# Optimization experiments

Hardware: AMD Instinct MI355X
Metric: run time of the kernel (lower is better)

Reference implementation:

```python
import jax, jax.numpy as jnp
import numpy as np


def setup_inputs() -> dict:
    key = jax.random.key(0)
    k1, k2, k3 = jax.random.split(key, 3)
    B, T, C, F = 32, 4096, 256, 256
    scale = 1.0 / np.sqrt(2 * C)  # glorot-ish fan-in scaling for kernel_size=2
    return {
        "x": jax.random.normal(k1, (B, T, C), dtype=jnp.float32),
        "Wv": jax.random.normal(k2, (2, C, F), dtype=jnp.float32) * scale,
        "bv": jnp.zeros((F,), dtype=jnp.float32),
        "Wg": jax.random.normal(k3, (2, C, F), dtype=jnp.float32) * scale,
        "bg": jnp.zeros((F,), dtype=jnp.float32),
        "dilation": 4,
    }


def _causal_dilated_k2(x, W, b, d):
    # Causal Conv1D, kernel_size=2, dilation d: y[t] = x[t-d] @ W[0] + x[t] @ W[1] + b
    T = x.shape[1]
    x_prev = jnp.pad(x, ((0, 0), (d, 0), (0, 0)))[:, :T]  # left-pad with zeros
    return (jnp.einsum("btc,cf->btf", x_prev, W[0])
            + jnp.einsum("btc,cf->btf", x, W[1]) + b)


def reference(x, Wv, bv, Wg, bg, dilation):
    value = jnp.tanh(_causal_dilated_k2(x, Wv, bv, dilation))
    gate = jax.nn.sigmoid(_causal_dilated_k2(x, Wg, bg, dilation))
    activations = value * gate
    # gate_merge = Concatenate (channel axis by default in Keras for 3D tensors)
    return jnp.concatenate([activations, x], axis=-1)
```

## Files before the change

kernel.cpp:

```cpp
#include <hip/hip_runtime.h>
#include <hip/hip_bf16.h>
#include <cstdint>

#define B_    32
#define T_    4096
#define C_    256
#define BM    64
#define DMAX  16
#define NROWS (BM + DMAX)

typedef __attribute__((ext_vector_type(8))) short bf16x8;
typedef __attribute__((ext_vector_type(4))) float f32x4;
typedef __attribute__((ext_vector_type(4))) short s16x4;

static __device__ __forceinline__ short f2bf(float f) {
  union { float f; uint32_t u; } v; v.f = f;
  uint32_t u = v.u;
  return (short)((u + 0x7fffu + ((u >> 16) & 1u)) >> 16);
}

__global__ void prep_weights(const float* __restrict__ Wv, const float* __restrict__ Wg,
                             const float* __restrict__ bv, const float* __restrict__ bg,
                             short* __restrict__ wimg, float* __restrict__ bcat) {
  int id = blockIdx.x * 256 + threadIdx.x;
  int kk = id & 31;
  int np = (id >> 5) & 255;
  int ks = (id >> 13) & 15;
  int nb = id >> 17;
  int k = ks * 32 + kk, tap = k >> 8, kr = k & 255;
  int sel = np >> 7;
  int f = nb * 128 + (np & 127);
  const float* W = sel ? Wg : Wv;
  wimg[id] = f2bf(W[((size_t)tap * 256 + kr) * 256 + f]);
  if (id < 512) bcat[id] = (id < 256) ? bv[id] : bg[id - 256];
}

__global__ __launch_bounds__(256, 4) void snail_main(
    const float* __restrict__ x, const short* __restrict__ wimg,
    const float* __restrict__ bcat, const int* __restrict__ dptr,
    float* __restrict__ out) {
  __shared__ __align__(16) short lx[NROWS * C_];

  const int d = *dptr;
  const int bid = blockIdx.x;
  const int swz = (bid & 7) * 512 + (bid >> 3);
  const int nb = swz & 1;
  const int t0 = ((swz >> 1) & 63) * BM;
  const int b  = swz >> 7;

  const int tid  = threadIdx.x;
  const int lane = tid & 63;
  const int w    = tid >> 6;
  const int row15 = lane & 15;
  const int qw    = lane >> 4;

  const float* xb = x + (size_t)b * T_ * C_;
  float* ob = out + (size_t)b * T_ * 512;

  for (int i = tid; i < d * 64; i += 256) {
    int r = i >> 6, c4 = i & 63;
    int t = t0 - d + r;
    f32x4 v = (f32x4){0.f, 0.f, 0.f, 0.f};
    if (t >= 0) v = *(const f32x4*)(xb + (size_t)t * C_ + c4 * 4);
    s16x4 s;
    s.x = f2bf(v.x); s.y = f2bf(v.y); s.z = f2bf(v.z); s.w = f2bf(v.w);
    int byte = (r * 512 + c4 * 8) ^ ((r & 7) << 4);
    *(s16x4*)((char*)lx + byte) = s;
  }
#pragma unroll 4
  for (int ii = 0; ii < 16; ++ii) {
    int i = ii * 256 + tid;
    int rr = i >> 6, c4 = i & 63;
    int t = t0 + rr, r = rr + d;
    f32x4 v = *(const f32x4*)(xb + (size_t)t * C_ + c4 * 4);
    if ((c4 >> 5) == nb)
      __builtin_nontemporal_store(v, (f32x4*)(ob + (size_t)t * 512 + C_ + c4 * 4));
    s16x4 s;
    s.x = f2bf(v.x); s.y = f2bf(v.y); s.z = f2bf(v.z); s.w = f2bf(v.w);
    int byte = (r * 512 + c4 * 8) ^ ((r & 7) << 4);
    *(s16x4*)((char*)lx + byte) = s;
  }
  __syncthreads();

  f32x4 accv[4][2], accg[4][2];
#pragma unroll
  for (int mi = 0; mi < 4; ++mi)
#pragma unroll
    for (int ni = 0; ni < 2; ++ni) {
      accv[mi][ni] = (f32x4){0.f, 0.f, 0.f, 0.f};
      accg[mi][ni] = (f32x4){0.f, 0.f, 0.f, 0.f};
    }

  const short* wl = wimg + (size_t)nb * 131072 + (w * 32 + row15) * 32 + qw * 8;

  for (int ks = 0; ks < 16; ++ks) {
    const short* wk = wl + ks * 8192;
    bf16x8 b0 = *(const bf16x8*)(wk);
    bf16x8 b1 = *(const bf16x8*)(wk + 512);
    bf16x8 g0 = *(const bf16x8*)(wk + 4096);
    bf16x8 g1 = *(const bf16x8*)(wk + 4608);

    bf16x8 af[4];
    const int rofs = (ks >= 8) ? d : 0;
    const int cb = (ks & 7) * 64 + qw * 16;
#pragma unroll
    for (int mi = 0; mi < 4; ++mi) {
      int r = 16 * mi + row15 + rofs;
      af[mi] = *(const bf16x8*)((const char*)lx + ((r * 512 + cb) ^ ((r & 7) << 4)));
    }
#pragma unroll
    for (int mi = 0; mi < 4; ++mi) {
      accv[mi][0] = __builtin_amdgcn_mfma_f32_16x16x32_bf16(b0, af[mi], accv[mi][0], 0, 0, 0);
      accv[mi][1] = __builtin_amdgcn_mfma_f32_16x16x32_bf16(b1, af[mi], accv[mi][1], 0, 0, 0);
      accg[mi][0] = __builtin_amdgcn_mfma_f32_16x16x32_bf16(g0, af[mi], accg[mi][0], 0, 0, 0);
      accg[mi][1] = __builtin_amdgcn_mfma_f32_16x16x32_bf16(g1, af[mi], accg[mi][1], 0, 0, 0);
    }
  }

#pragma unroll
  for (int ni = 0; ni < 2; ++ni) {
    int f0 = nb * 128 + w * 32 + 16 * ni + qw * 4;
    f32x4 bv4 = *(const f32x4*)(bcat + f0);
    f32x4 bg4 = *(const f32x4*)(bcat + 256 + f0);
#pragma unroll
    for (int mi = 0; mi < 4; ++mi) {
      int t = t0 + 16 * mi + row15;
      f32x4 v = accv[mi][ni], g = accg[mi][ni];
      f32x4 res;
#pragma unroll
      for (int j = 0; j < 4; ++j) {
        float vv = v[j] + bv4[j], gg = g[j] + bg4[j];
        float th = 1.f - 2.f / (__expf(2.f * vv) + 1.f);
        float sg = 1.f / (1.f + __expf(-gg));
        res[j] = th * sg;
      }
      __builtin_nontemporal_store(res, (f32x4*)(ob + (size_t)t * 512 + f0));
    }
  }
}

extern "C" void kernel_launch(void* const* d_in, const int* in_sizes, int n_in,
                              void* d_out, int out_size, void* d_ws, size_t ws_size,
                              hipStream_t stream) {
  const float* x  = (const float*)d_in[0];
  const float* Wv = (const float*)d_in[1];
  const float* bv = (const float*)d_in[2];
  const float* Wg = (const float*)d_in[3];
  const float* bg = (const float*)d_in[4];
  const int* dil  = (const int*)d_in[5];
  float* out = (float*)d_out;

  short* wimg = (short*)d_ws;
  float* bcat = (float*)((char*)d_ws + 16 * 32768);

  prep_weights<<<1024, 256, 0, stream>>>(Wv, Wg, bv, bg, wimg, bcat);
  snail_main<<<B_ * (T_ / BM) * 2, 256, 0, stream>>>(x, wimg, bcat, dil, out);
}
```

Before: 127.8 us.

## Cover all 256 output features per block with 512 threads, merge x load loops

Each block now computes the full 512-wide value/gate output for a 64-row tile using 8 waves in a 2x4 arrangement, instead of two blocks each handling half of the features. This halves the x tile loading and bf16 conversion into LDS, which were previously duplicated across the two feature halves, and merges the halo and main load loops into one. It also swaps the divisions in tanh/sigmoid for hardware reciprocal and uses the library bf16 conversion. The trade-offs are fewer, larger blocks and more register pressure from 8 weight fragments per k-step under launch_bounds(512,4).

```diff
diff --git a/kernel.cpp b/kernel.cpp
--- a/kernel.cpp
+++ b/kernel.cpp
@@ -14,9 +14,13 @@
 typedef __attribute__((ext_vector_type(4))) short s16x4;
 
 static __device__ __forceinline__ short f2bf(float f) {
-  union { float f; uint32_t u; } v; v.f = f;
-  uint32_t u = v.u;
-  return (short)((u + 0x7fffu + ((u >> 16) & 1u)) >> 16);
+  __hip_bfloat16 h = __float2bfloat16(f);
+  union { __hip_bfloat16 h; short s; } u; u.h = h;
+  return u.s;
+}
+
+static __device__ __forceinline__ float rcp_(float x) {
+  return __builtin_amdgcn_rcpf(x);
 }
 
 __global__ void prep_weights(const float* __restrict__ Wv, const float* __restrict__ Wg,
@@ -35,7 +39,7 @@
   if (id < 512) bcat[id] = (id < 256) ? bv[id] : bg[id - 256];
 }
 
-__global__ __launch_bounds__(256, 4) void snail_main(
+__global__ __launch_bounds__(512, 4) void snail_main(
     const float* __restrict__ x, const short* __restrict__ wimg,
     const float* __restrict__ bcat, const int* __restrict__ dptr,
     float* __restrict__ out) {
@@ -43,37 +47,28 @@
 
   const int d = *dptr;
   const int bid = blockIdx.x;
-  const int swz = (bid & 7) * 512 + (bid >> 3);
-  const int nb = swz & 1;
-  const int t0 = ((swz >> 1) & 63) * BM;
-  const int b  = swz >> 7;
+  const int swz = (bid & 7) * 256 + (bid >> 3);
+  const int t0 = (swz & 63) * BM;
+  const int b  = swz >> 6;
 
   const int tid  = threadIdx.x;
   const int lane = tid & 63;
   const int w    = tid >> 6;
+  const int wm   = w >> 2;
+  const int wn   = w & 3;
   const int row15 = lane & 15;
   const int qw    = lane >> 4;
 
   const float* xb = x + (size_t)b * T_ * C_;
   float* ob = out + (size_t)b * T_ * 512;
 
-  for (int i = tid; i < d * 64; i += 256) {
+  const int nrows = BM + d;
+  for (int i = tid; i < nrows * 64; i += 512) {
     int r = i >> 6, c4 = i & 63;
     int t = t0 - d + r;
     f32x4 v = (f32x4){0.f, 0.f, 0.f, 0.f};
     if (t >= 0) v = *(const f32x4*)(xb + (size_t)t * C_ + c4 * 4);
-    s16x4 s;
-    s.x = f2bf(v.x); s.y = f2bf(v.y); s.z = f2bf(v.z); s.w = f2bf(v.w);
-    int byte = (r * 512 + c4 * 8) ^ ((r & 7) << 4);
-    *(s16x4*)((char*)lx + byte) = s;
-  }
-#pragma unroll 4
-  for (int ii = 0; ii < 16; ++ii) {
-    int i = ii * 256 + tid;
-    int rr = i >> 6, c4 = i & 63;
-    int t = t0 + rr, r = rr + d;
-    f32x4 v = *(const f32x4*)(xb + (size_t)t * C_ + c4 * 4);
-    if ((c4 >> 5) == nb)
+    if (r >= d)
       __builtin_nontemporal_store(v, (f32x4*)(ob + (size_t)t * 512 + C_ + c4 * 4));
     s16x4 s;
     s.x = f2bf(v.x); s.y = f2bf(v.y); s.z = f2bf(v.z); s.w = f2bf(v.w);
@@ -82,56 +77,60 @@
   }
   __syncthreads();
 
-  f32x4 accv[4][2], accg[4][2];
+  f32x4 accv[2][4], accg[2][4];
 #pragma unroll
-  for (int mi = 0; mi < 4; ++mi)
+  for (int mi = 0; mi < 2; ++mi)
 #pragma unroll
-    for (int ni = 0; ni < 2; ++ni) {
+    for (int ni = 0; ni < 4; ++ni) {
       accv[mi][ni] = (f32x4){0.f, 0.f, 0.f, 0.f};
       accg[mi][ni] = (f32x4){0.f, 0.f, 0.f, 0.f};
     }
 
-  const short* wl = wimg + (size_t)nb * 131072 + (w * 32 + row15) * 32 + qw * 8;
+  const short* wl = wimg + (size_t)(wn >> 1) * 131072 +
+                    ((wn & 1) * 64 + row15) * 32 + qw * 8;
 
+#pragma unroll 2
   for (int ks = 0; ks < 16; ++ks) {
     const short* wk = wl + ks * 8192;
-    bf16x8 b0 = *(const bf16x8*)(wk);
-    bf16x8 b1 = *(const bf16x8*)(wk + 512);
-    bf16x8 g0 = *(const bf16x8*)(wk + 4096);
-    bf16x8 g1 = *(const bf16x8*)(wk + 4608);
+    bf16x8 wv_[4], wg_[4];
+#pragma unroll
+    for (int ni = 0; ni < 4; ++ni) {
+      wv_[ni] = *(const bf16x8*)(wk + ni * 512);
+      wg_[ni] = *(const bf16x8*)(wk + ni * 512 + 4096);
+    }
 
-    bf16x8 af[4];
+    bf16x8 af[2];
     const int rofs = (ks >= 8) ? d : 0;
     const int cb = (ks & 7) * 64 + qw * 16;
 #pragma unroll
-    for (int mi = 0; mi < 4; ++mi) {
-      int r = 16 * mi + row15 + rofs;
+    for (int mi = 0; mi < 2; ++mi) {
+      int r = 32 * wm + 16 * mi + row15 + rofs;
       af[mi] = *(const bf16x8*)((const char*)lx + ((r * 512 + cb) ^ ((r & 7) << 4)));
     }
 #pragma unroll
-    for (int mi = 0; mi < 4; ++mi) {
-      accv[mi][0] = __builtin_amdgcn_mfma_f32_16x16x32_bf16(b0, af[mi], accv[mi][0], 0, 0, 0);
-      accv[mi][1] = __builtin_amdgcn_mfma_f32_16x16x32_bf16(b1, af[mi], accv[mi][1], 0, 0, 0);
-      accg[mi][0] = __builtin_amdgcn_mfma_f32_16x16x32_bf16(g0, af[mi], accg[mi][0], 0, 0, 0);
-      accg[mi][1] = __builtin_amdgcn_mfma_f32_16x16x32_bf16(g1, af[mi], accg[mi][1], 0, 0, 0);
-    }
+    for (int ni = 0; ni < 4; ++ni)
+#pragma unroll
+      for (int mi = 0; mi < 2; ++mi) {
+        accv[mi][ni] = __builtin_amdgcn_mfma_f32_16x16x32_bf16(wv_[ni], af[mi], accv[mi][ni], 0, 0, 0);
+        accg[mi][ni] = __builtin_amdgcn_mfma_f32_16x16x32_bf16(wg_[ni], af[mi], accg[mi][ni], 0, 0, 0);
+      }
   }
 
 #pragma unroll
-  for (int ni = 0; ni < 2; ++ni) {
-    int f0 = nb * 128 + w * 32 + 16 * ni + qw * 4;
+  for (int ni = 0; ni < 4; ++ni) {
+    int f0 = 64 * wn + 16 * ni + qw * 4;
     f32x4 bv4 = *(const f32x4*)(bcat + f0);
     f32x4 bg4 = *(const f32x4*)(bcat + 256 + f0);
 #pragma unroll
-    for (int mi = 0; mi < 4; ++mi) {
-      int t = t0 + 16 * mi + row15;
+    for (int mi = 0; mi < 2; ++mi) {
+      int t = t0 + 32 * wm + 16 * mi + row15;
       f32x4 v = accv[mi][ni], g = accg[mi][ni];
       f32x4 res;
 #pragma unroll
       for (int j = 0; j < 4; ++j) {
         float vv = v[j] + bv4[j], gg = g[j] + bg4[j];
-        float th = 1.f - 2.f / (__expf(2.f * vv) + 1.f);
-        float sg = 1.f / (1.f + __expf(-gg));
+        float th = 1.f - 2.f * rcp_(__expf(2.f * vv) + 1.f);
+        float sg = rcp_(1.f + __expf(-gg));
         res[j] = th * sg;
       }
       __builtin_nontemporal_store(res, (f32x4*)(ob + (size_t)t * 512 + f0));
@@ -154,5 +153,5 @@
   float* bcat = (float*)((char*)d_ws + 16 * 32768);
 
   prep_weights<<<1024, 256, 0, stream>>>(Wv, Wg, bv, bg, wimg, bcat);
-  snail_main<<<B_ * (T_ / BM) * 2, 256, 0, stream>>>(x, wimg, bcat, dil, out);
+  snail_main<<<B_ * (T_ / BM), 512, 0, stream>>>(x, wimg, bcat, dil, out);
 }
```

After: 179.2 us. 1.4x slower.
